# Kernel optimization log

Hardware: AMD Instinct MI355X
Metric: run time of the kernel (lower is better)

Reference implementation:

```python
import jax, jax.numpy as jnp
import numpy as np

B, S = 1, 2048
H, KV, D = 32, 8, 128          # query heads, kv heads, head_size
G = H // KV                     # num_queries_per_kv (GQA group size)
SCALE = 1.0 / float(np.sqrt(D))


def setup_inputs() -> dict:
    key = jax.random.key(0)
    k1, k2, k3 = jax.random.split(key, 3)
    slopes = jnp.asarray(2.0 ** (-8.0 * np.arange(1, H + 1) / H), dtype=jnp.float32)
    return {
        "query": jax.random.normal(k1, (B, S, H * D), dtype=jnp.float32),
        "key": jax.random.normal(k2, (B, S, KV * D), dtype=jnp.float32),
        "value": jax.random.normal(k3, (B, S, KV * D), dtype=jnp.float32),
        "alibi_slopes": slopes,
    }


def reference(query, key, value, alibi_slopes):
    b, s, _ = query.shape
    # [B,S,H*D] -> [B,KV,G,S,D] (GQA unflatten of query heads into kv groups)
    q = query.reshape(b, s, KV, G, D).transpose(0, 2, 3, 1, 4)
    k = key.reshape(b, s, KV, D).transpose(0, 2, 1, 3)      # [B,KV,S,D]
    v = value.reshape(b, s, KV, D).transpose(0, 2, 1, 3)    # [B,KV,S,D]

    # _make_alibi_bias: bias[i,j] = (j - i) * slope_h, then unflatten heads to (KV, G)
    pos = jnp.arange(s)
    rel = (pos[None, :] - pos[:, None]).astype(query.dtype)         # [S,S]
    bias = alibi_slopes[:, None, None] * rel                        # [H,S,S]
    causal = jnp.where(pos[None, :] > pos[:, None], -jnp.inf, 0.0).astype(query.dtype)
    bias = (bias + causal).reshape(KV, G, s, s)                     # [KV,G,S,S]

    # scaled QK^T + bias, softmax, AV (non-fused prompt_attention path)
    scores = jnp.einsum('bkgsd,bktd->bkgst', q * SCALE, k) + bias   # [B,KV,G,S,S]
    probs = jax.nn.softmax(scores, axis=-1)
    out = jnp.einsum('bkgst,bktd->bkgsd', probs, v)                 # [B,KV,G,S,D]
    # flatten (KV,G) -> H and back to [B,S,H*D]
    return out.transpose(0, 3, 1, 2, 4).reshape(b, s, H * D)
```

## Files before the change

### kernel.cpp

```cpp
#include <hip/hip_runtime.h>
#include <hip/hip_bf16.h>

#define S_LEN 2048
#define NHEADS 32
#define NKV 8
#define HD 128
#define QK_SCALE 0.08838834764831845f
#define LOG2E 1.4426950408889634f
#define QK_SCALE2 (QK_SCALE * LOG2E)
#define DTHR 11.5416f

#define BQ 64
#define BK 32
#define NQT (S_LEN / BQ)
#define QSTR (NHEADS * HD)
#define KSTR (NKV * HD)

#define K_STRIDE 136
#define VT_STRIDE 40
#define P_STRIDE 40

typedef __attribute__((ext_vector_type(8))) short bf16x8;
typedef __attribute__((ext_vector_type(4))) float f32x4;
typedef __attribute__((ext_vector_type(4))) unsigned u32x4;
typedef __attribute__((ext_vector_type(2))) unsigned u32x2;

__device__ inline unsigned cvt_pk_bf16(float lo, float hi) {
    unsigned r;
    asm("v_cvt_pk_bf16_f32 %0, %1, %2" : "=v"(r) : "v"(lo), "v"(hi));
    return r;
}
__device__ inline bf16x8 as_bf16x8(u32x4 v) {
    union { u32x4 u; bf16x8 b; } c; c.u = v; return c.b;
}

__global__ __launch_bounds__(256) void attn_fwd(
    const float* __restrict__ Q, const float* __restrict__ K,
    const float* __restrict__ V, const float* __restrict__ SL,
    float* __restrict__ O)
{
    const int bx   = blockIdx.x;
    const int h    = bx & (NHEADS - 1);
    const int qt   = (NQT - 1) - (bx >> 5);
    const int kvh  = h >> 2;
    const float slope  = SL[h];
    const float slope2 = slope * LOG2E;

    const int tid  = threadIdx.x;
    const int w    = tid >> 6;
    const int lane = tid & 63;
    const int l16  = lane & 15;
    const int lq   = lane >> 4;

    __shared__ short Ks[2][BK * K_STRIDE];
    __shared__ short VTs[2][HD * VT_STRIDE];
    __shared__ short Ps[4][16 * P_STRIDE];

    const int qrow0 = qt * BQ + w * 16;
    const int q     = qrow0 + l16;

    bf16x8 qf[4];
    {
        const float* qp = Q + (size_t)q * QSTR + h * HD + lq * 8;
        #pragma unroll
        for (int d0 = 0; d0 < 4; ++d0) {
            f32x4 a = *(const f32x4*)(qp + d0 * 32);
            f32x4 b = *(const f32x4*)(qp + d0 * 32 + 4);
            u32x4 t;
            t[0] = cvt_pk_bf16(a[0] * QK_SCALE2, a[1] * QK_SCALE2);
            t[1] = cvt_pk_bf16(a[2] * QK_SCALE2, a[3] * QK_SCALE2);
            t[2] = cvt_pk_bf16(b[0] * QK_SCALE2, b[1] * QK_SCALE2);
            t[3] = cvt_pk_bf16(b[2] * QK_SCALE2, b[3] * QK_SCALE2);
            qf[d0] = as_bf16x8(t);
        }
    }

    f32x4 acc[8];
    #pragma unroll
    for (int t = 0; t < 8; ++t) acc[t] = (f32x4){0.f, 0.f, 0.f, 0.f};
    float m_ = -1e30f, l_ = 0.f;

    const int kv_end = qt * BQ + BQ;
    int kb_start = 0;
    {
        float th = (float)(qt * BQ) - 31.0f - 45.0f / slope;
        int t = (int)floorf(th);
        kb_start = (t < 0) ? 0 : (((t >> 5) + 1) << 5);
    }

    const int sr  = tid >> 4, scc = tid & 15;
    const int vd  = tid & 127, vrb = (tid >> 7) * 8;
    const float* Kbase = K + (size_t)kvh * HD + scc * 8;
    const float* Vbase = V + (size_t)kvh * HD + vd;

    float kr[2][8], vr[2][8];

    auto load_regs = [&](int kb) {
        #pragma unroll
        for (int s = 0; s < 2; ++s) {
            const float* kp = Kbase + (size_t)(kb + sr + s * 16) * KSTR;
            *(f32x4*)&kr[s][0] = *(const f32x4*)kp;
            *(f32x4*)&kr[s][4] = *(const f32x4*)(kp + 4);
        }
        #pragma unroll
        for (int s = 0; s < 2; ++s)
            #pragma unroll
            for (int j = 0; j < 8; ++j)
                vr[s][j] = Vbase[(size_t)(kb + vrb + s * 16 + j) * KSTR];
    };

    auto store_tile = [&](int b) {
        #pragma unroll
        for (int s = 0; s < 2; ++s) {
            u32x4 t;
            t[0] = cvt_pk_bf16(kr[s][0], kr[s][1]);
            t[1] = cvt_pk_bf16(kr[s][2], kr[s][3]);
            t[2] = cvt_pk_bf16(kr[s][4], kr[s][5]);
            t[3] = cvt_pk_bf16(kr[s][6], kr[s][7]);
            *(u32x4*)&Ks[b][(sr + s * 16) * K_STRIDE + scc * 8] = t;
        }
        #pragma unroll
        for (int s = 0; s < 2; ++s) {
            u32x4 t;
            t[0] = cvt_pk_bf16(vr[s][0], vr[s][1]);
            t[1] = cvt_pk_bf16(vr[s][2], vr[s][3]);
            t[2] = cvt_pk_bf16(vr[s][4], vr[s][5]);
            t[3] = cvt_pk_bf16(vr[s][6], vr[s][7]);
            *(u32x4*)&VTs[b][vd * VT_STRIDE + vrb + s * 16] = t;
        }
    };

    load_regs(kb_start);
    store_tile(0);
    int cur = 0;

    for (int kb = kb_start; kb < kv_end; kb += BK) {
        asm volatile("s_waitcnt lgkmcnt(0)\n\ts_barrier" ::: "memory");

        const bool has_next = (kb + BK) < kv_end;
        if (has_next) load_regs(kb + BK);

        const bool live = (kb <= qrow0 + 15) &&
                          (slope * (float)(qrow0 - kb - 31) < 45.0f);
        if (live) {
            const short* Kc = &Ks[cur][0];
            const short* Vc = &VTs[cur][0];

            f32x4 sc0 = (f32x4){0.f,0.f,0.f,0.f};
            f32x4 sc1 = (f32x4){0.f,0.f,0.f,0.f};
            #pragma unroll
            for (int d0 = 0; d0 < 4; ++d0) {
                bf16x8 kf0 = *(const bf16x8*)&Kc[l16 * K_STRIDE + d0 * 32 + lq * 8];
                bf16x8 kf1 = *(const bf16x8*)&Kc[(16 + l16) * K_STRIDE + d0 * 32 + lq * 8];
                sc0 = __builtin_amdgcn_mfma_f32_16x16x32_bf16(kf0, qf[d0], sc0, 0, 0, 0);
                sc1 = __builtin_amdgcn_mfma_f32_16x16x32_bf16(kf1, qf[d0], sc1, 0, 0, 0);
            }

            const int kq0 = kb + 4 * lq - q;
            float s[8];
            #pragma unroll
            for (int i = 0; i < 4; ++i) {
                int d0i = kq0 + i, d1i = kq0 + 16 + i;
                float b0 = __builtin_fmaf(slope2, (float)d0i, sc0[i]);
                float b1 = __builtin_fmaf(slope2, (float)d1i, sc1[i]);
                s[i]     = (d0i > 0) ? -1e30f : b0;
                s[i + 4] = (d1i > 0) ? -1e30f : b1;
            }

            float rm = fmaxf(fmaxf(fmaxf(s[0], s[1]), fmaxf(s[2], s[3])),
                             fmaxf(fmaxf(s[4], s[5]), fmaxf(s[6], s[7])));
            rm = fmaxf(rm, __shfl_xor(rm, 16));
            rm = fmaxf(rm, __shfl_xor(rm, 32));

            bool need = (rm > m_ + DTHR);
            if (__any(need)) {
                float mn    = need ? rm : m_;
                float alpha = exp2f(m_ - mn);
                m_ = mn;
                l_ *= alpha;
                #pragma unroll
                for (int t = 0; t < 8; ++t) {
                    acc[t][0] *= alpha; acc[t][1] *= alpha;
                    acc[t][2] *= alpha; acc[t][3] *= alpha;
                }
            }

            float p[8];
            #pragma unroll
            for (int j = 0; j < 8; ++j) p[j] = exp2f(s[j] - m_);
            float ts = ((p[0] + p[1]) + (p[2] + p[3])) +
                       ((p[4] + p[5]) + (p[6] + p[7]));
            ts += __shfl_xor(ts, 16);
            ts += __shfl_xor(ts, 32);
            l_ += ts;

            u32x2 pa, pb;
            pa[0] = cvt_pk_bf16(p[0], p[1]); pa[1] = cvt_pk_bf16(p[2], p[3]);
            pb[0] = cvt_pk_bf16(p[4], p[5]); pb[1] = cvt_pk_bf16(p[6], p[7]);

            short* PsW = &Ps[w][0];
            *(u32x2*)&PsW[l16 * P_STRIDE + 4 * lq]      = pa;
            *(u32x2*)&PsW[l16 * P_STRIDE + 16 + 4 * lq] = pb;
            asm volatile("s_waitcnt lgkmcnt(0)" ::: "memory");
            bf16x8 pf = *(const bf16x8*)&PsW[l16 * P_STRIDE + lq * 8];

            #pragma unroll
            for (int nt = 0; nt < 8; ++nt) {
                bf16x8 vf = *(const bf16x8*)&Vc[(nt * 16 + l16) * VT_STRIDE + lq * 8];
                acc[nt] = __builtin_amdgcn_mfma_f32_16x16x32_bf16(vf, pf, acc[nt], 0, 0, 0);
            }
        }

        if (has_next) store_tile(cur ^ 1);
        cur ^= 1;
    }

    {
        float rl = 1.0f / l_;
        float* op = O + (size_t)q * QSTR + h * HD + 4 * lq;
        #pragma unroll
        for (int nt = 0; nt < 8; ++nt) {
            f32x4 o = acc[nt];
            o[0] *= rl; o[1] *= rl; o[2] *= rl; o[3] *= rl;
            *(f32x4*)(op + nt * 16) = o;
        }
    }
}

extern "C" void kernel_launch(void* const* d_in, const int* in_sizes, int n_in,
                              void* d_out, int out_size, void* d_ws, size_t ws_size,
                              hipStream_t stream) {
    const float* Q  = (const float*)d_in[0];
    const float* K  = (const float*)d_in[1];
    const float* V  = (const float*)d_in[2];
    const float* SL = (const float*)d_in[3];
    float* O = (float*)d_out;

    dim3 grid(NQT * NHEADS);
    dim3 block(256);
    attn_fwd<<<grid, block, 0, stream>>>(Q, K, V, SL, O);
}
```

Baseline: 102.3 us.

## Precompute bf16 K and transposed bf16 V in workspace before attention

Adds two pre-pass kernels: one converts K to bf16 in a head-major layout, the other converts V to bf16 and transposes it through shared memory. The attention kernel then loads 16-byte bf16 vectors instead of fp32 values, including the strided scalar V loads. This removes repeated per-block fp32 loads and conversions of K/V across the many query tiles sharing a kv head. The cost is two extra launches and a workspace round trip. An unused f2bf helper is also added.

```diff
diff --git a/kernel.cpp b/kernel.cpp
--- a/kernel.cpp
+++ b/kernel.cpp
@@ -30,13 +30,58 @@
     asm("v_cvt_pk_bf16_f32 %0, %1, %2" : "=v"(r) : "v"(lo), "v"(hi));
     return r;
 }
+__device__ inline short f2bf(float f) {
+    unsigned u = __float_as_uint(f);
+    u += 0x7fffu + ((u >> 16) & 1u);
+    return (short)(u >> 16);
+}
 __device__ inline bf16x8 as_bf16x8(u32x4 v) {
     union { u32x4 u; bf16x8 b; } c; c.u = v; return c.b;
 }
 
+__global__ __launch_bounds__(256) void prep_k(const float* __restrict__ K,
+                                              short* __restrict__ Kbf) {
+    int g = blockIdx.x * 256 + threadIdx.x;
+    int chunk = g & 15, kvh = (g >> 4) & 7, s = g >> 7;
+    const float* in = K + (size_t)s * KSTR + kvh * HD + chunk * 8;
+    f32x4 a = *(const f32x4*)in;
+    f32x4 b = *(const f32x4*)(in + 4);
+    u32x4 t;
+    t[0] = cvt_pk_bf16(a[0], a[1]); t[1] = cvt_pk_bf16(a[2], a[3]);
+    t[2] = cvt_pk_bf16(b[0], b[1]); t[3] = cvt_pk_bf16(b[2], b[3]);
+    *(u32x4*)(Kbf + ((size_t)kvh * S_LEN + s) * HD + chunk * 8) = t;
+}
+
+__global__ __launch_bounds__(256) void prep_v(const float* __restrict__ V,
+                                              short* __restrict__ Vtb) {
+    __shared__ short Ts[64][72];
+    int b = blockIdx.x;
+    int sb = b & 31, db = (b >> 5) & 1, kvh = b >> 6;
+    int t = threadIdx.x, r = t >> 2, c0 = (t & 3) * 16;
+
+    const float* in = V + (size_t)(sb * 64 + r) * KSTR + kvh * HD + db * 64 + c0;
+    f32x4 a0 = *(const f32x4*)in,        a1 = *(const f32x4*)(in + 4);
+    f32x4 a2 = *(const f32x4*)(in + 8),  a3 = *(const f32x4*)(in + 12);
+    u32x4 t0;
+    t0[0] = cvt_pk_bf16(a0[0], a0[1]); t0[1] = cvt_pk_bf16(a0[2], a0[3]);
+    t0[2] = cvt_pk_bf16(a1[0], a1[1]); t0[3] = cvt_pk_bf16(a1[2], a1[3]);
+    *(u32x4*)&Ts[r][c0] = t0;
+    t0[0] = cvt_pk_bf16(a2[0], a2[1]); t0[1] = cvt_pk_bf16(a2[2], a2[3]);
+    t0[2] = cvt_pk_bf16(a3[0], a3[1]); t0[3] = cvt_pk_bf16(a3[2], a3[3]);
+    *(u32x4*)&Ts[r][c0 + 8] = t0;
+    __syncthreads();
+
+    alignas(16) short tmp[16];
+    #pragma unroll
+    for (int j = 0; j < 16; ++j) tmp[j] = Ts[c0 + j][r];
+    short* dst = Vtb + ((size_t)(kvh * HD + db * 64 + r)) * S_LEN + sb * 64 + c0;
+    *(u32x4*)dst       = *(u32x4*)&tmp[0];
+    *(u32x4*)(dst + 8) = *(u32x4*)&tmp[8];
+}
+
 __global__ __launch_bounds__(256) void attn_fwd(
-    const float* __restrict__ Q, const float* __restrict__ K,
-    const float* __restrict__ V, const float* __restrict__ SL,
+    const float* __restrict__ Q, const short* __restrict__ Kbf,
+    const short* __restrict__ Vtb, const float* __restrict__ SL,
     float* __restrict__ O)
 {
     const int bx   = blockIdx.x;
@@ -47,8 +92,8 @@
     const float slope2 = slope * LOG2E;
 
     const int tid  = threadIdx.x;
+    const int lane = tid & 63;
     const int w    = tid >> 6;
-    const int lane = tid & 63;
     const int l16  = lane & 15;
     const int lq   = lane >> 4;
 
@@ -90,44 +135,27 @@
 
     const int sr  = tid >> 4, scc = tid & 15;
     const int vd  = tid & 127, vrb = (tid >> 7) * 8;
-    const float* Kbase = K + (size_t)kvh * HD + scc * 8;
-    const float* Vbase = V + (size_t)kvh * HD + vd;
-
-    float kr[2][8], vr[2][8];
+    const short* Kst = Kbf + (size_t)kvh * S_LEN * HD + scc * 8;
+    const short* Vst = Vtb + (size_t)(kvh * HD + vd) * S_LEN;
+
+    u32x4 kreg[2], vreg[2];
 
     auto load_regs = [&](int kb) {
         #pragma unroll
-        for (int s = 0; s < 2; ++s) {
-            const float* kp = Kbase + (size_t)(kb + sr + s * 16) * KSTR;
-            *(f32x4*)&kr[s][0] = *(const f32x4*)kp;
-            *(f32x4*)&kr[s][4] = *(const f32x4*)(kp + 4);
-        }
-        #pragma unroll
-        for (int s = 0; s < 2; ++s)
-            #pragma unroll
-            for (int j = 0; j < 8; ++j)
-                vr[s][j] = Vbase[(size_t)(kb + vrb + s * 16 + j) * KSTR];
+        for (int s = 0; s < 2; ++s)
+            kreg[s] = *(const u32x4*)(Kst + (size_t)(kb + sr + s * 16) * HD);
+        #pragma unroll
+        for (int s = 0; s < 2; ++s)
+            vreg[s] = *(const u32x4*)(Vst + kb + vrb + s * 16);
     };
 
     auto store_tile = [&](int b) {
         #pragma unroll
-        for (int s = 0; s < 2; ++s) {
-            u32x4 t;
-            t[0] = cvt_pk_bf16(kr[s][0], kr[s][1]);
-            t[1] = cvt_pk_bf16(kr[s][2], kr[s][3]);
-            t[2] = cvt_pk_bf16(kr[s][4], kr[s][5]);
-            t[3] = cvt_pk_bf16(kr[s][6], kr[s][7]);
-            *(u32x4*)&Ks[b][(sr + s * 16) * K_STRIDE + scc * 8] = t;
-        }
-        #pragma unroll
-        for (int s = 0; s < 2; ++s) {
-            u32x4 t;
-            t[0] = cvt_pk_bf16(vr[s][0], vr[s][1]);
-            t[1] = cvt_pk_bf16(vr[s][2], vr[s][3]);
-            t[2] = cvt_pk_bf16(vr[s][4], vr[s][5]);
-            t[3] = cvt_pk_bf16(vr[s][6], vr[s][7]);
-            *(u32x4*)&VTs[b][vd * VT_STRIDE + vrb + s * 16] = t;
-        }
+        for (int s = 0; s < 2; ++s)
+            *(u32x4*)&Ks[b][(sr + s * 16) * K_STRIDE + scc * 8] = kreg[s];
+        #pragma unroll
+        for (int s = 0; s < 2; ++s)
+            *(u32x4*)&VTs[b][vd * VT_STRIDE + vrb + s * 16] = vreg[s];
     };
 
     load_regs(kb_start);
@@ -236,7 +264,10 @@
     const float* SL = (const float*)d_in[3];
     float* O = (float*)d_out;
 
-    dim3 grid(NQT * NHEADS);
-    dim3 block(256);
-    attn_fwd<<<grid, block, 0, stream>>>(Q, K, V, SL, O);
-}
+    short* Kbf = (short*)d_ws;
+    short* Vtb = (short*)d_ws + (size_t)NKV * S_LEN * HD;
+
+    prep_k<<<dim3(1024), dim3(256), 0, stream>>>(K, Kbf);
+    prep_v<<<dim3(512),  dim3(256), 0, stream>>>(V, Vtb);
+    attn_fwd<<<dim3(NQT * NHEADS), dim3(256), 0, stream>>>(Q, Kbf, Vtb, SL, O);
+}
```

Measured after the change: 96.89 us. -5.3%, faster.
